# Kernel optimization log

Measured on AMD Instinct MI355X. Metric: run time of the kernel, lower is better.

## Reference

```python
import math
import jax, jax.numpy as jnp
import numpy as np

B, S, D_MODEL, H = 2, 2048, 1024, 16
D_HEAD = D_MODEL // H
NEG = -90000000000.0


def setup_inputs() -> dict:
    key = jax.random.key(0)
    ks = jax.random.split(key, 12)
    scale = 1.0 / math.sqrt(D_MODEL)
    return {
        "Q": jax.random.normal(ks[0], (B, S, D_MODEL), jnp.float32),
        "K": jax.random.normal(ks[1], (B, S, D_MODEL), jnp.float32),
        "V": jax.random.normal(ks[2], (B, S, D_MODEL), jnp.float32),
        "mask": jax.random.randint(ks[3], (B, 1, S, S), 0, 2).astype(bool),
        "Wq": jax.random.normal(ks[4], (D_MODEL, D_MODEL), jnp.float32) * scale,
        "bq": jnp.zeros((D_MODEL,), jnp.float32),
        "Wk": jax.random.normal(ks[5], (D_MODEL, D_MODEL), jnp.float32) * scale,
        "bk": jnp.zeros((D_MODEL,), jnp.float32),
        "Wv": jax.random.normal(ks[6], (D_MODEL, D_MODEL), jnp.float32) * scale,
        "bv": jnp.zeros((D_MODEL,), jnp.float32),
        "Wo": jax.random.normal(ks[7], (D_MODEL, D_MODEL), jnp.float32) * scale,
        "bo": jnp.zeros((D_MODEL,), jnp.float32),
    }


def _split_heads(x):
    # (B, S, D) -> (B, H, S, Dh)
    b, s, _ = x.shape
    return x.reshape(b, s, H, D_HEAD).transpose(0, 2, 1, 3)


def reference(Q, K, V, mask, Wq, bq, Wk, bk, Wv, bv, Wo, bo):
    q = _split_heads(Q @ Wq.T + bq)
    k = _split_heads(K @ Wk.T + bk)
    v = _split_heads(V @ Wv.T + bv)
    # scaled dot product with additive mask (mask.float() * -9e10)
    scores = jnp.einsum("bhqd,bhkd->bhqk", q, k) / math.sqrt(D_HEAD)
    scores = scores + mask.astype(scores.dtype) * NEG
    attn = jax.nn.softmax(scores, axis=-1)
    ctx = jnp.einsum("bhqk,bhkd->bhqd", attn, v)  # (B, H, S, Dh)
    ctx = ctx.transpose(0, 2, 1, 3).reshape(Q.shape[0], q.shape[2], D_MODEL)
    return ctx @ Wo.T + bo
```

## Files before the change

kernel.cpp:

```cpp
#include <hip/hip_runtime.h>
#include <hip/hip_bf16.h>


typedef __bf16 bf16x8 __attribute__((ext_vector_type(8)));
typedef float f32x4 __attribute__((ext_vector_type(4)));

#define S_LEN 2048
#define DM 1024
#define NH 16
#define DH 64
#define MROWS 4096

static __device__ __forceinline__ unsigned short f2bf(float f) {
    __hip_bfloat16 h = __float2bfloat16(f);
    unsigned short u; __builtin_memcpy(&u, &h, 2); return u;
}

static __device__ __forceinline__ bf16x8 cvt8(float4 a, float4 b) {
    bf16x8 o;
    o[0] = (__bf16)a.x; o[1] = (__bf16)a.y; o[2] = (__bf16)a.z; o[3] = (__bf16)a.w;
    o[4] = (__bf16)b.x; o[5] = (__bf16)b.y; o[6] = (__bf16)b.z; o[7] = (__bf16)b.w;
    return o;
}

__global__ __launch_bounds__(256)
void cvt3(const float* __restrict__ s0, unsigned short* __restrict__ d0,
          const float* __restrict__ s1, unsigned short* __restrict__ d1,
          const float* __restrict__ s2, unsigned short* __restrict__ d2, int n)
{
    const float* s = blockIdx.y == 0 ? s0 : blockIdx.y == 1 ? s1 : s2;
    unsigned short* d = blockIdx.y == 0 ? d0 : blockIdx.y == 1 ? d1 : d2;
    int i = (blockIdx.x * 256 + threadIdx.x) * 8;
    if (i < n) {
        float4 a = *(const float4*)(s + i);
        float4 b = *(const float4*)(s + i + 4);
        *(bf16x8*)(d + i) = cvt8(a, b);
    }
}

__global__ __launch_bounds__(256)
void pack_mask(const int* __restrict__ m, unsigned* __restrict__ mb)
{
    const int lane = threadIdx.x & 63, w = threadIdx.x >> 6;
    const int row = blockIdx.x * 4 + w;
    const int* src = m + (size_t)row * S_LEN;
    unsigned* dst = mb + (size_t)row * (S_LEN / 32);
    for (int i = 0; i < 32; i++) {
        int v = src[i * 64 + lane];
        unsigned long long bm = __ballot(v != 0);
        if (lane == 0) { dst[i * 2] = (unsigned)bm; dst[i * 2 + 1] = (unsigned)(bm >> 32); }
    }
}

__global__ __launch_bounds__(256)
void gemm128(const unsigned short* __restrict__ X0, const unsigned short* __restrict__ X1,
             const unsigned short* __restrict__ X2,
             const unsigned short* __restrict__ W0, const unsigned short* __restrict__ W1,
             const unsigned short* __restrict__ W2,
             const float* __restrict__ b0, const float* __restrict__ b1,
             const float* __restrict__ b2,
             unsigned short* __restrict__ d0, unsigned short* __restrict__ d1,
             unsigned short* __restrict__ d2, float* __restrict__ dstf, int mode_base)
{
    __shared__ __align__(16) unsigned short As[128 * 32];
    __shared__ __align__(16) unsigned short Bs[128 * 32];
    const int z = blockIdx.z;
    const unsigned short* X = z == 0 ? X0 : z == 1 ? X1 : X2;
    const unsigned short* W = z == 0 ? W0 : z == 1 ? W1 : W2;
    const float* bias        = z == 0 ? b0 : z == 1 ? b1 : b2;
    unsigned short* dstb     = z == 0 ? d0 : z == 1 ? d1 : d2;
    const int mode = mode_base + z;

    const int tid  = threadIdx.x;
    const int m0   = blockIdx.y * 128;
    const int n0   = blockIdx.x * 128;
    const int lane = tid & 63;
    const int w    = tid >> 6;
    const int wm   = (w >> 1) * 64, wn = (w & 1) * 64;
    const int lr   = lane & 15;
    const int lg   = lane >> 4;

    f32x4 acc[4][4];
#pragma unroll
    for (int i = 0; i < 4; i++)
#pragma unroll
        for (int j = 0; j < 4; j++) acc[i][j] = f32x4{0.f, 0.f, 0.f, 0.f};

    for (int k0 = 0; k0 < DM; k0 += 32) {
        __syncthreads();
#pragma unroll
        for (int j = 0; j < 2; j++) {
            int e = tid + j * 256;
            int row = e >> 2, c8 = (e & 3) * 8;
            __builtin_amdgcn_global_load_lds(
                (const __attribute__((address_space(1))) unsigned*)&X[(size_t)(m0 + row) * DM + k0 + c8],
                (__attribute__((address_space(3))) unsigned*)&As[e * 8], 16, 0, 0);
            __builtin_amdgcn_global_load_lds(
                (const __attribute__((address_space(1))) unsigned*)&W[(size_t)(n0 + row) * DM + k0 + c8],
                (__attribute__((address_space(3))) unsigned*)&Bs[e * 8], 16, 0, 0);
        }
        __syncthreads();
        bf16x8 af[4], bfr[4];
#pragma unroll
        for (int mi = 0; mi < 4; mi++)
            af[mi] = *(const bf16x8*)(&As[(wm + mi * 16 + lr) * 32 + lg * 8]);
#pragma unroll
        for (int ni = 0; ni < 4; ni++)
            bfr[ni] = *(const bf16x8*)(&Bs[(wn + ni * 16 + lr) * 32 + lg * 8]);
#pragma unroll
        for (int mi = 0; mi < 4; mi++)
#pragma unroll
            for (int ni = 0; ni < 4; ni++)
                acc[mi][ni] = __builtin_amdgcn_mfma_f32_16x16x32_bf16(
                    af[mi], bfr[ni], acc[mi][ni], 0, 0, 0);
    }

#pragma unroll
    for (int mi = 0; mi < 4; mi++) {
#pragma unroll
        for (int ni = 0; ni < 4; ni++) {
            const int gcol = n0 + wn + ni * 16 + lr;
            const float bv = bias[gcol];
            const int grow0 = m0 + wm + mi * 16 + lg * 4;
            if (mode == 2) {
                int b = grow0 >> 11, s = grow0 & (S_LEN - 1);
                int h = gcol >> 6, dh = gcol & 63;
                unsigned short us[4];
#pragma unroll
                for (int r = 0; r < 4; r++) us[r] = f2bf(acc[mi][ni][r] + bv);
                size_t di = ((size_t)(b * NH + h) * DH + dh) * S_LEN + s;
                *(ushort2*)(&d2[di])     = ushort2{us[0], us[1]};
                *(ushort2*)(&d2[di + 2]) = ushort2{us[2], us[3]};
            } else {
#pragma unroll
                for (int r = 0; r < 4; r++) {
                    int grow = grow0 + r;
                    float v = acc[mi][ni][r] + bv;
                    if (mode == 3) {
                        dstf[(size_t)grow * DM + gcol] = v;
                    } else {
                        int b = grow >> 11, s = grow & (S_LEN - 1);
                        int h = gcol >> 6, dh = gcol & 63;
                        dstb[((size_t)(b * NH + h) * S_LEN + s) * DH + dh] = f2bf(v);
                    }
                }
            }
        }
    }
}

__global__ __launch_bounds__(256, 4)
void attn(const unsigned short* __restrict__ q_ws,
          const unsigned short* __restrict__ k_ws,
          const unsigned short* __restrict__ vt_ws,
          const unsigned* __restrict__ mbits,
          unsigned short* __restrict__ ctx)
{
    __shared__ __align__(16) unsigned short Ks[64 * 72];
    __shared__ __align__(16) unsigned short Vs[64 * 72];
    __shared__ __align__(16) unsigned short P_lds[4][16 * 72];
    const int tid = threadIdx.x, lane = tid & 63, w = tid >> 6;
    const int lr = lane & 15, lg = lane >> 4;

    const int i    = blockIdx.x;
    const int xcd  = i & 7;
    const int slot = i >> 3;
    const int bh   = xcd * 4 + (slot >> 5);
    const int qblk = slot & 31;
    const int b  = bh >> 4;
    const int h  = bh & 15;
    const int q0 = qblk * 64 + w * 16;

    const int srow = tid >> 3;
    const int sseg = tid & 7;

    const unsigned short* qh = q_ws + (size_t)bh * S_LEN * DH;
    const unsigned short* kh = k_ws + (size_t)bh * S_LEN * DH;
    const unsigned short* vh = vt_ws + (size_t)bh * DH * S_LEN;
    const unsigned* mrow = mbits + (size_t)(b * S_LEN) * (S_LEN / 32);

    bf16x8 aq[2];
#pragma unroll
    for (int c = 0; c < 2; c++)
        aq[c] = *(const bf16x8*)(&qh[(size_t)(q0 + lr) * DH + c * 32 + lg * 8]);

    f32x4 acc[4];
#pragma unroll
    for (int di = 0; di < 4; di++) acc[di] = f32x4{0.f, 0.f, 0.f, 0.f};
    float rs[4] = {0.f, 0.f, 0.f, 0.f};

    uint4 kreg0, kreg1, vreg0, vreg1;
    kreg0 = *(const uint4*)(&kh[(size_t)(srow)      * DH + sseg * 8]);
    kreg1 = *(const uint4*)(&kh[(size_t)(srow + 32) * DH + sseg * 8]);
    vreg0 = *(const uint4*)(&vh[(size_t)(srow)      * S_LEN + sseg * 8]);
    vreg1 = *(const uint4*)(&vh[(size_t)(srow + 32) * S_LEN + sseg * 8]);

    for (int it = 0; it < 32; it++) {
        const int kv0 = it * 64;
        __syncthreads();
        *(uint4*)(&Ks[(srow)      * 72 + sseg * 8]) = kreg0;
        *(uint4*)(&Ks[(srow + 32) * 72 + sseg * 8]) = kreg1;
        *(uint4*)(&Vs[(srow)      * 72 + sseg * 8]) = vreg0;
        *(uint4*)(&Vs[(srow + 32) * 72 + sseg * 8]) = vreg1;
        __syncthreads();
        if (it < 31) {
            const int kn = kv0 + 64;
            kreg0 = *(const uint4*)(&kh[(size_t)(kn + srow)      * DH + sseg * 8]);
            kreg1 = *(const uint4*)(&kh[(size_t)(kn + srow + 32) * DH + sseg * 8]);
            vreg0 = *(const uint4*)(&vh[(size_t)(srow)      * S_LEN + kn + sseg * 8]);
            vreg1 = *(const uint4*)(&vh[(size_t)(srow + 32) * S_LEN + kn + sseg * 8]);
        }

        uint2 mw[4];
#pragma unroll
        for (int r = 0; r < 4; r++)
            mw[r] = *(const uint2*)(&mrow[(size_t)(q0 + lg * 4 + r) * (S_LEN / 32) + (kv0 >> 5)]);

        f32x4 sf[4];
#pragma unroll
        for (int ni = 0; ni < 4; ni++) {
            bf16x8 bk0 = *(const bf16x8*)(&Ks[(ni * 16 + lr) * 72 + lg * 8]);
            bf16x8 bk1 = *(const bf16x8*)(&Ks[(ni * 16 + lr) * 72 + 32 + lg * 8]);
            f32x4 t = __builtin_amdgcn_mfma_f32_16x16x32_bf16(aq[0], bk0, f32x4{0.f,0.f,0.f,0.f}, 0,0,0);
            t = __builtin_amdgcn_mfma_f32_16x16x32_bf16(aq[1], bk1, t, 0,0,0);
            sf[ni] = t;
        }
#pragma unroll
        for (int ni = 0; ni < 4; ni++)
#pragma unroll
            for (int r = 0; r < 4; r++) {
                unsigned word = (ni & 2) ? mw[r].y : mw[r].x;
                unsigned bit = (word >> ((ni & 1) * 16 + lr)) & 1u;
                float t = sf[ni][r] * 0.125f + (bit ? -1e5f : -8.0f);
                float p = __expf(fminf(t, 60.f));
                sf[ni][r] = p;
                rs[r] += p;
            }

        unsigned short* pl_ = &P_lds[w][0];
#pragma unroll
        for (int ni = 0; ni < 4; ni++)
#pragma unroll
            for (int r = 0; r < 4; r++)
                pl_[(lg * 4 + r) * 72 + ni * 16 + lr] = f2bf(sf[ni][r]);

        bf16x8 ap0 = *(const bf16x8*)(&pl_[lr * 72 + lg * 8]);
        bf16x8 ap1 = *(const bf16x8*)(&pl_[lr * 72 + 32 + lg * 8]);
#pragma unroll
        for (int di = 0; di < 4; di++) {
            bf16x8 bv0 = *(const bf16x8*)(&Vs[(di * 16 + lr) * 72 + lg * 8]);
            bf16x8 bv1 = *(const bf16x8*)(&Vs[(di * 16 + lr) * 72 + 32 + lg * 8]);
            acc[di] = __builtin_amdgcn_mfma_f32_16x16x32_bf16(ap0, bv0, acc[di], 0, 0, 0);
            acc[di] = __builtin_amdgcn_mfma_f32_16x16x32_bf16(ap1, bv1, acc[di], 0, 0, 0);
        }
    }

    float inv[4];
#pragma unroll
    for (int r = 0; r < 4; r++) {
        float v = rs[r];
        v += __shfl_xor(v, 1);
        v += __shfl_xor(v, 2);
        v += __shfl_xor(v, 4);
        v += __shfl_xor(v, 8);
        inv[r] = 1.0f / fmaxf(v, 1e-37f);
    }
#pragma unroll
    for (int di = 0; di < 4; di++)
#pragma unroll
        for (int r = 0; r < 4; r++) {
            int qrow = q0 + lg * 4 + r;
            ctx[((size_t)(b * S_LEN + qrow)) * DM + h * DH + di * 16 + lr] =
                f2bf(acc[di][r] * inv[r]);
        }
}

extern "C" void kernel_launch(void* const* d_in, const int* in_sizes, int n_in,
                              void* d_out, int out_size, void* d_ws, size_t ws_size,
                              hipStream_t stream)
{
    (void)in_sizes; (void)n_in; (void)out_size; (void)ws_size;
    const float* Q  = (const float*)d_in[0];
    const float* K  = (const float*)d_in[1];
    const float* V  = (const float*)d_in[2];
    const int*   Mk = (const int*)d_in[3];
    const float* Wq = (const float*)d_in[4];
    const float* bq = (const float*)d_in[5];
    const float* Wk = (const float*)d_in[6];
    const float* bk = (const float*)d_in[7];
    const float* Wv = (const float*)d_in[8];
    const float* bv = (const float*)d_in[9];
    const float* Wo = (const float*)d_in[10];
    const float* bo = (const float*)d_in[11];

    const int NX = MROWS * DM;
    const int NW = DM * DM;

    unsigned short* q_ws  = (unsigned short*)d_ws;
    unsigned short* k_ws  = q_ws + (size_t)NX;
    unsigned short* vt_ws = k_ws + (size_t)NX;
    unsigned short* ctx   = vt_ws + (size_t)NX;
    unsigned*       mbits = (unsigned*)(ctx + (size_t)NX);
    unsigned short* Wbq   = (unsigned short*)(mbits + (size_t)MROWS * (S_LEN / 32));
    unsigned short* Wbk   = Wbq + (size_t)NW;
    unsigned short* Wbv   = Wbk + (size_t)NW;
    unsigned short* Wbo   = Wbv + (size_t)NW;
    unsigned short* Xbq   = Wbo + (size_t)NW;
    unsigned short* Xbk   = Xbq + (size_t)NX;
    unsigned short* Xbv   = Xbk + (size_t)NX;
    float* out = (float*)d_out;

    dim3 blk(256);
    pack_mask<<<dim3(1024), blk, 0, stream>>>(Mk, mbits);
    cvt3<<<dim3(2048, 3), blk, 0, stream>>>(Q, Xbq, K, Xbk, V, Xbv, NX);
    cvt3<<<dim3(512, 3), blk, 0, stream>>>(Wq, Wbq, Wk, Wbk, Wv, Wbv, NW);
    cvt3<<<dim3(512, 1), blk, 0, stream>>>(Wo, Wbo, nullptr, nullptr, nullptr, nullptr, NW);

    gemm128<<<dim3(8, 32, 3), blk, 0, stream>>>(Xbq, Xbk, Xbv, Wbq, Wbk, Wbv,
                                                bq, bk, bv, q_ws, k_ws, vt_ws,
                                                nullptr, 0);

    attn<<<dim3(1024), blk, 0, stream>>>(q_ws, k_ws, vt_ws, mbits, ctx);

    gemm128<<<dim3(8, 32, 1), blk, 0, stream>>>(ctx, nullptr, nullptr, Wbo, nullptr, nullptr,
                                                bo, nullptr, nullptr, nullptr, nullptr, nullptr,
                                                out, 3);
}
```

Baseline: 303.7 us.

## Fuse prep kernels, transpose attention MFMA operands, add smaller-tile output GEMM

Merges the mask packing and the four fp32->bf16 conversion launches into a single prep kernel to cut launch overhead. In attention, the MFMA operands are swapped so each lane owns one query row: the mask becomes one uint2 load per row, the row sum needs only two shuffles, and P and ctx are written as packed 8-byte stores. The output projection moves to a dedicated 128x64-tile GEMM, doubling the block count to 512 for better CU occupancy. The V-transpose store is also packed into one uint2 write.

```diff
diff --git a/kernel.cpp b/kernel.cpp
--- a/kernel.cpp
+++ b/kernel.cpp
@@ -24,31 +24,44 @@
 }
 
 __global__ __launch_bounds__(256)
-void cvt3(const float* __restrict__ s0, unsigned short* __restrict__ d0,
-          const float* __restrict__ s1, unsigned short* __restrict__ d1,
-          const float* __restrict__ s2, unsigned short* __restrict__ d2, int n)
-{
-    const float* s = blockIdx.y == 0 ? s0 : blockIdx.y == 1 ? s1 : s2;
-    unsigned short* d = blockIdx.y == 0 ? d0 : blockIdx.y == 1 ? d1 : d2;
-    int i = (blockIdx.x * 256 + threadIdx.x) * 8;
-    if (i < n) {
+void prep(const int* __restrict__ m, unsigned* __restrict__ mb,
+          const float* __restrict__ Q, unsigned short* __restrict__ dQ,
+          const float* __restrict__ K, unsigned short* __restrict__ dK,
+          const float* __restrict__ V, unsigned short* __restrict__ dV,
+          const float* __restrict__ W0, unsigned short* __restrict__ dW0,
+          const float* __restrict__ W1, unsigned short* __restrict__ dW1,
+          const float* __restrict__ W2, unsigned short* __restrict__ dW2,
+          const float* __restrict__ W3, unsigned short* __restrict__ dW3)
+{
+    const int bx = blockIdx.x, tid = threadIdx.x;
+    if (bx < 1024) {
+        const int lane = tid & 63, w = tid >> 6;
+        const int row = bx * 4 + w;
+        const int* src = m + (size_t)row * S_LEN;
+        unsigned* dst = mb + (size_t)row * (S_LEN / 32);
+        for (int i = 0; i < 32; i++) {
+            int v = src[i * 64 + lane];
+            unsigned long long bm = __ballot(v != 0);
+            if (lane == 0) { dst[i*2] = (unsigned)bm; dst[i*2+1] = (unsigned)(bm >> 32); }
+        }
+    } else if (bx < 7168) {
+        int t = bx - 1024;
+        int which = t >> 11;
+        const float* s = which == 0 ? Q : which == 1 ? K : V;
+        unsigned short* d = which == 0 ? dQ : which == 1 ? dK : dV;
+        int i = ((t & 2047) * 256 + tid) * 8;
         float4 a = *(const float4*)(s + i);
         float4 b = *(const float4*)(s + i + 4);
         *(bf16x8*)(d + i) = cvt8(a, b);
-    }
-}
-
-__global__ __launch_bounds__(256)
-void pack_mask(const int* __restrict__ m, unsigned* __restrict__ mb)
-{
-    const int lane = threadIdx.x & 63, w = threadIdx.x >> 6;
-    const int row = blockIdx.x * 4 + w;
-    const int* src = m + (size_t)row * S_LEN;
-    unsigned* dst = mb + (size_t)row * (S_LEN / 32);
-    for (int i = 0; i < 32; i++) {
-        int v = src[i * 64 + lane];
-        unsigned long long bm = __ballot(v != 0);
-        if (lane == 0) { dst[i * 2] = (unsigned)bm; dst[i * 2 + 1] = (unsigned)(bm >> 32); }
+    } else {
+        int t = bx - 7168;
+        int which = t >> 9;
+        const float* s = which == 0 ? W0 : which == 1 ? W1 : which == 2 ? W2 : W3;
+        unsigned short* d = which == 0 ? dW0 : which == 1 ? dW1 : which == 2 ? dW2 : dW3;
+        int i = ((t & 511) * 256 + tid) * 8;
+        float4 a = *(const float4*)(s + i);
+        float4 b = *(const float4*)(s + i + 4);
+        *(bf16x8*)(d + i) = cvt8(a, b);
     }
 }
 
@@ -60,7 +73,7 @@
              const float* __restrict__ b0, const float* __restrict__ b1,
              const float* __restrict__ b2,
              unsigned short* __restrict__ d0, unsigned short* __restrict__ d1,
-             unsigned short* __restrict__ d2, float* __restrict__ dstf, int mode_base)
+             unsigned short* __restrict__ d2)
 {
     __shared__ __align__(16) unsigned short As[128 * 32];
     __shared__ __align__(16) unsigned short Bs[128 * 32];
@@ -69,7 +82,6 @@
     const unsigned short* W = z == 0 ? W0 : z == 1 ? W1 : W2;
     const float* bias        = z == 0 ? b0 : z == 1 ? b1 : b2;
     unsigned short* dstb     = z == 0 ? d0 : z == 1 ? d1 : d2;
-    const int mode = mode_base + z;
 
     const int tid  = threadIdx.x;
     const int m0   = blockIdx.y * 128;
@@ -122,31 +134,93 @@
             const int gcol = n0 + wn + ni * 16 + lr;
             const float bv = bias[gcol];
             const int grow0 = m0 + wm + mi * 16 + lg * 4;
-            if (mode == 2) {
+            if (z == 2) {
                 int b = grow0 >> 11, s = grow0 & (S_LEN - 1);
                 int h = gcol >> 6, dh = gcol & 63;
                 unsigned short us[4];
 #pragma unroll
                 for (int r = 0; r < 4; r++) us[r] = f2bf(acc[mi][ni][r] + bv);
                 size_t di = ((size_t)(b * NH + h) * DH + dh) * S_LEN + s;
-                *(ushort2*)(&d2[di])     = ushort2{us[0], us[1]};
-                *(ushort2*)(&d2[di + 2]) = ushort2{us[2], us[3]};
+                unsigned lo = (unsigned)us[0] | ((unsigned)us[1] << 16);
+                unsigned hi = (unsigned)us[2] | ((unsigned)us[3] << 16);
+                *(uint2*)(&dstb[di]) = uint2{lo, hi};
             } else {
 #pragma unroll
                 for (int r = 0; r < 4; r++) {
                     int grow = grow0 + r;
                     float v = acc[mi][ni][r] + bv;
-                    if (mode == 3) {
-                        dstf[(size_t)grow * DM + gcol] = v;
-                    } else {
-                        int b = grow >> 11, s = grow & (S_LEN - 1);
-                        int h = gcol >> 6, dh = gcol & 63;
-                        dstb[((size_t)(b * NH + h) * S_LEN + s) * DH + dh] = f2bf(v);
-                    }
+                    int b = grow >> 11, s = grow & (S_LEN - 1);
+                    int h = gcol >> 6, dh = gcol & 63;
+                    dstb[((size_t)(b * NH + h) * S_LEN + s) * DH + dh] = f2bf(v);
                 }
             }
         }
     }
+}
+
+__global__ __launch_bounds__(256)
+void gemm_out(const unsigned short* __restrict__ X, const unsigned short* __restrict__ W,
+              const float* __restrict__ bias, float* __restrict__ dst)
+{
+    __shared__ __align__(16) unsigned short As[128 * 32];
+    __shared__ __align__(16) unsigned short Bs[64 * 32];
+    const int tid  = threadIdx.x;
+    const int m0   = blockIdx.y * 128;
+    const int n0   = blockIdx.x * 64;
+    const int lane = tid & 63;
+    const int w    = tid >> 6;
+    const int wm   = (w >> 1) * 64, wn = (w & 1) * 32;
+    const int lr   = lane & 15;
+    const int lg   = lane >> 4;
+
+    f32x4 acc[4][2];
+#pragma unroll
+    for (int i = 0; i < 4; i++)
+#pragma unroll
+        for (int j = 0; j < 2; j++) acc[i][j] = f32x4{0.f, 0.f, 0.f, 0.f};
+
+    for (int k0 = 0; k0 < DM; k0 += 32) {
+        __syncthreads();
+#pragma unroll
+        for (int j = 0; j < 2; j++) {
+            int e = tid + j * 256;
+            int row = e >> 2, c8 = (e & 3) * 8;
+            __builtin_amdgcn_global_load_lds(
+                (const __attribute__((address_space(1))) unsigned*)&X[(size_t)(m0 + row) * DM + k0 + c8],
+                (__attribute__((address_space(3))) unsigned*)&As[e * 8], 16, 0, 0);
+        }
+        {
+            int row = tid >> 2, c8 = (tid & 3) * 8;
+            __builtin_amdgcn_global_load_lds(
+                (const __attribute__((address_space(1))) unsigned*)&W[(size_t)(n0 + row) * DM + k0 + c8],
+                (__attribute__((address_space(3))) unsigned*)&Bs[tid * 8], 16, 0, 0);
+        }
+        __syncthreads();
+        bf16x8 af[4], bfr[2];
+#pragma unroll
+        for (int mi = 0; mi < 4; mi++)
+            af[mi] = *(const bf16x8*)(&As[(wm + mi * 16 + lr) * 32 + lg * 8]);
+#pragma unroll
+        for (int ni = 0; ni < 2; ni++)
+            bfr[ni] = *(const bf16x8*)(&Bs[(wn + ni * 16 + lr) * 32 + lg * 8]);
+#pragma unroll
+        for (int mi = 0; mi < 4; mi++)
+#pragma unroll
+            for (int ni = 0; ni < 2; ni++)
+                acc[mi][ni] = __builtin_amdgcn_mfma_f32_16x16x32_bf16(
+                    af[mi], bfr[ni], acc[mi][ni], 0, 0, 0);
+    }
+#pragma unroll
+    for (int mi = 0; mi < 4; mi++)
+#pragma unroll
+        for (int ni = 0; ni < 2; ni++) {
+            const int gcol = n0 + wn + ni * 16 + lr;
+            const float bv = bias[gcol];
+            const int grow0 = m0 + wm + mi * 16 + lg * 4;
+#pragma unroll
+            for (int r = 0; r < 4; r++)
+                dst[(size_t)(grow0 + r) * DM + gcol] = acc[mi][ni][r] + bv;
+        }
 }
 
 __global__ __launch_bounds__(256, 4)
@@ -158,7 +232,7 @@
 {
     __shared__ __align__(16) unsigned short Ks[64 * 72];
     __shared__ __align__(16) unsigned short Vs[64 * 72];
-    __shared__ __align__(16) unsigned short P_lds[4][16 * 72];
+    __shared__ __align__(16) unsigned short Pq[4][16 * 72];
     const int tid = threadIdx.x, lane = tid & 63, w = tid >> 6;
     const int lr = lane & 15, lg = lane >> 4;
 
@@ -170,6 +244,7 @@
     const int b  = bh >> 4;
     const int h  = bh & 15;
     const int q0 = qblk * 64 + w * 16;
+    const int qrow = q0 + lr;
 
     const int srow = tid >> 3;
     const int sseg = tid & 7;
@@ -177,17 +252,17 @@
     const unsigned short* qh = q_ws + (size_t)bh * S_LEN * DH;
     const unsigned short* kh = k_ws + (size_t)bh * S_LEN * DH;
     const unsigned short* vh = vt_ws + (size_t)bh * DH * S_LEN;
-    const unsigned* mrow = mbits + (size_t)(b * S_LEN) * (S_LEN / 32);
+    const unsigned* mrow = mbits + (size_t)(b * S_LEN + qrow) * (S_LEN / 32);
 
     bf16x8 aq[2];
 #pragma unroll
     for (int c = 0; c < 2; c++)
-        aq[c] = *(const bf16x8*)(&qh[(size_t)(q0 + lr) * DH + c * 32 + lg * 8]);
+        aq[c] = *(const bf16x8*)(&qh[(size_t)qrow * DH + c * 32 + lg * 8]);
 
     f32x4 acc[4];
 #pragma unroll
     for (int di = 0; di < 4; di++) acc[di] = f32x4{0.f, 0.f, 0.f, 0.f};
-    float rs[4] = {0.f, 0.f, 0.f, 0.f};
+    float rs = 0.f;
 
     uint4 kreg0, kreg1, vreg0, vreg1;
     kreg0 = *(const uint4*)(&kh[(size_t)(srow)      * DH + sseg * 8]);
@@ -211,68 +286,59 @@
             vreg1 = *(const uint4*)(&vh[(size_t)(srow + 32) * S_LEN + kn + sseg * 8]);
         }
 
-        uint2 mw[4];
-#pragma unroll
-        for (int r = 0; r < 4; r++)
-            mw[r] = *(const uint2*)(&mrow[(size_t)(q0 + lg * 4 + r) * (S_LEN / 32) + (kv0 >> 5)]);
+        const uint2 mw = *(const uint2*)(&mrow[kv0 >> 5]);
 
         f32x4 sf[4];
 #pragma unroll
         for (int ni = 0; ni < 4; ni++) {
-            bf16x8 bk0 = *(const bf16x8*)(&Ks[(ni * 16 + lr) * 72 + lg * 8]);
-            bf16x8 bk1 = *(const bf16x8*)(&Ks[(ni * 16 + lr) * 72 + 32 + lg * 8]);
-            f32x4 t = __builtin_amdgcn_mfma_f32_16x16x32_bf16(aq[0], bk0, f32x4{0.f,0.f,0.f,0.f}, 0,0,0);
-            t = __builtin_amdgcn_mfma_f32_16x16x32_bf16(aq[1], bk1, t, 0,0,0);
+            bf16x8 ak0 = *(const bf16x8*)(&Ks[(ni * 16 + lr) * 72 + lg * 8]);
+            bf16x8 ak1 = *(const bf16x8*)(&Ks[(ni * 16 + lr) * 72 + 32 + lg * 8]);
+            f32x4 t = __builtin_amdgcn_mfma_f32_16x16x32_bf16(ak0, aq[0], f32x4{0.f,0.f,0.f,0.f}, 0,0,0);
+            t = __builtin_amdgcn_mfma_f32_16x16x32_bf16(ak1, aq[1], t, 0,0,0);
             sf[ni] = t;
         }
 #pragma unroll
         for (int ni = 0; ni < 4; ni++)
 #pragma unroll
             for (int r = 0; r < 4; r++) {
-                unsigned word = (ni & 2) ? mw[r].y : mw[r].x;
-                unsigned bit = (word >> ((ni & 1) * 16 + lr)) & 1u;
+                unsigned word = (ni & 2) ? mw.y : mw.x;
+                unsigned bit = (word >> ((ni & 1) * 16 + lg * 4 + r)) & 1u;
                 float t = sf[ni][r] * 0.125f + (bit ? -1e5f : -8.0f);
                 float p = __expf(fminf(t, 60.f));
                 sf[ni][r] = p;
-                rs[r] += p;
+                rs += p;
             }
 
-        unsigned short* pl_ = &P_lds[w][0];
-#pragma unroll
-        for (int ni = 0; ni < 4; ni++)
-#pragma unroll
-            for (int r = 0; r < 4; r++)
-                pl_[(lg * 4 + r) * 72 + ni * 16 + lr] = f2bf(sf[ni][r]);
-
-        bf16x8 ap0 = *(const bf16x8*)(&pl_[lr * 72 + lg * 8]);
-        bf16x8 ap1 = *(const bf16x8*)(&pl_[lr * 72 + 32 + lg * 8]);
+        unsigned short* pq = &Pq[w][0];
+#pragma unroll
+        for (int ni = 0; ni < 4; ni++) {
+            unsigned lo = (unsigned)f2bf(sf[ni][0]) | ((unsigned)f2bf(sf[ni][1]) << 16);
+            unsigned hi = (unsigned)f2bf(sf[ni][2]) | ((unsigned)f2bf(sf[ni][3]) << 16);
+            *(uint2*)(&pq[lr * 72 + ni * 16 + lg * 4]) = uint2{lo, hi};
+        }
+
+        bf16x8 bp0 = *(const bf16x8*)(&pq[lr * 72 + lg * 8]);
+        bf16x8 bp1 = *(const bf16x8*)(&pq[lr * 72 + 32 + lg * 8]);
 #pragma unroll
         for (int di = 0; di < 4; di++) {
-            bf16x8 bv0 = *(const bf16x8*)(&Vs[(di * 16 + lr) * 72 + lg * 8]);
-            bf16x8 bv1 = *(const bf16x8*)(&Vs[(di * 16 + lr) * 72 + 32 + lg * 8]);
-            acc[di] = __builtin_amdgcn_mfma_f32_16x16x32_bf16(ap0, bv0, acc[di], 0, 0, 0);
-            acc[di] = __builtin_amdgcn_mfma_f32_16x16x32_bf16(ap1, bv1, acc[di], 0, 0, 0);
-        }
-    }
-
-    float inv[4];
-#pragma unroll
-    for (int r = 0; r < 4; r++) {
-        float v = rs[r];
-        v += __shfl_xor(v, 1);
-        v += __shfl_xor(v, 2);
-        v += __shfl_xor(v, 4);
-        v += __shfl_xor(v, 8);
-        inv[r] = 1.0f / fmaxf(v, 1e-37f);
-    }
-#pragma unroll
-    for (int di = 0; di < 4; di++)
-#pragma unroll
-        for (int r = 0; r < 4; r++) {
-            int qrow = q0 + lg * 4 + r;
-            ctx[((size_t)(b * S_LEN + qrow)) * DM + h * DH + di * 16 + lr] =
-                f2bf(acc[di][r] * inv[r]);
-        }
+            bf16x8 av0 = *(const bf16x8*)(&Vs[(di * 16 + lr) * 72 + lg * 8]);
+            bf16x8 av1 = *(const bf16x8*)(&Vs[(di * 16 + lr) * 72 + 32 + lg * 8]);
+            acc[di] = __builtin_amdgcn_mfma_f32_16x16x32_bf16(av0, bp0, acc[di], 0, 0, 0);
+            acc[di] = __builtin_amdgcn_mfma_f32_16x16x32_bf16(av1, bp1, acc[di], 0, 0, 0);
+        }
+    }
+
+    rs += __shfl_xor(rs, 16);
+    rs += __shfl_xor(rs, 32);
+    const float inv = 1.0f / fmaxf(rs, 1e-37f);
+
+    unsigned short* crow = &ctx[((size_t)(b * S_LEN + qrow)) * DM + h * DH];
+#pragma unroll
+    for (int di = 0; di < 4; di++) {
+        unsigned lo = (unsigned)f2bf(acc[di][0] * inv) | ((unsigned)f2bf(acc[di][1] * inv) << 16);
+        unsigned hi = (unsigned)f2bf(acc[di][2] * inv) | ((unsigned)f2bf(acc[di][3] * inv) << 16);
+        *(uint2*)(&crow[di * 16 + lg * 4]) = uint2{lo, hi};
+    }
 }
 
 extern "C" void kernel_launch(void* const* d_in, const int* in_sizes, int n_in,
@@ -311,18 +377,13 @@
     float* out = (float*)d_out;
 
     dim3 blk(256);
-    pack_mask<<<dim3(1024), blk, 0, stream>>>(Mk, mbits);
-    cvt3<<<dim3(2048, 3), blk, 0, stream>>>(Q, Xbq, K, Xbk, V, Xbv, NX);
-    cvt3<<<dim3(512, 3), blk, 0, stream>>>(Wq, Wbq, Wk, Wbk, Wv, Wbv, NW);
-    cvt3<<<dim3(512, 1), blk, 0, stream>>>(Wo, Wbo, nullptr, nullptr, nullptr, nullptr, NW);
+    prep<<<dim3(9216), blk, 0, stream>>>(Mk, mbits, Q, Xbq, K, Xbk, V, Xbv,
+                                         Wq, Wbq, Wk, Wbk, Wv, Wbv, Wo, Wbo);
 
     gemm128<<<dim3(8, 32, 3), blk, 0, stream>>>(Xbq, Xbk, Xbv, Wbq, Wbk, Wbv,
-                                                bq, bk, bv, q_ws, k_ws, vt_ws,
-                                                nullptr, 0);
+                                                bq, bk, bv, q_ws, k_ws, vt_ws);
 
     attn<<<dim3(1024), blk, 0, stream>>>(q_ws, k_ws, vt_ws, mbits, ctx);
 
-    gemm128<<<dim3(8, 32, 1), blk, 0, stream>>>(ctx, nullptr, nullptr, Wbo, nullptr, nullptr,
-                                                bo, nullptr, nullptr, nullptr, nullptr, nullptr,
-                                                out, 3);
-}
+    gemm_out<<<dim3(16, 32), blk, 0, stream>>>(ctx, Wbo, bo, out);
+}
```

Measured after the change: 280.9 us. -7.5%, faster.
